# Kernel optimization log

Measured on AMD Instinct MI355X. Metric: run time of the kernel, lower is better.

## Reference

```python
import jax, jax.numpy as jnp
import numpy as np

D = 1024      # neural_dim
M = 8192      # memory_size (assumed fully used)
H = 16        # num_heads
B = 64        # batch
HD = D // H   # head dim


def setup_inputs() -> dict:
    key = jax.random.key(0)
    ks = jax.random.split(key, 24)
    s = 0.02
    inp = {
        "neural_input": jax.random.normal(ks[0], (B, D), jnp.float32),
        "memory_keys": jax.random.normal(ks[1], (M, D), jnp.float32),
        "memory_values": jax.random.normal(ks[2], (M, D), jnp.float32),
        # query/key/value projections (nn.Linear weights are [out, in])
        "Wq": jax.random.normal(ks[3], (D, D), jnp.float32) * s,
        "bq": jnp.zeros((D,), jnp.float32),
        "Wk": jax.random.normal(ks[4], (D, D), jnp.float32) * s,
        "bk": jnp.zeros((D,), jnp.float32),
        "Wv": jax.random.normal(ks[5], (D, D), jnp.float32) * s,
        "bv": jnp.zeros((D,), jnp.float32),
        # MultiheadAttention packed in-projection [3D, D] and out projection
        "in_proj_w": jax.random.normal(ks[6], (3 * D, D), jnp.float32) * s,
        "in_proj_b": jnp.zeros((3 * D,), jnp.float32),
        "out_w": jax.random.normal(ks[7], (D, D), jnp.float32) * s,
        "out_b": jnp.zeros((D,), jnp.float32),
        # memory_gate: Linear(2D->D), ReLU, Linear(D->D), Sigmoid
        "gW1": jax.random.normal(ks[8], (D, 2 * D), jnp.float32) * s,
        "gb1": jnp.zeros((D,), jnp.float32),
        "gW2": jax.random.normal(ks[9], (D, D), jnp.float32) * s,
        "gb2": jnp.zeros((D,), jnp.float32),
        # integration: Linear(2D->2D), ReLU, Linear(2D->D)
        "iW1": jax.random.normal(ks[10], (2 * D, 2 * D), jnp.float32) * s,
        "ib1": jnp.zeros((2 * D,), jnp.float32),
        "iW2": jax.random.normal(ks[11], (D, 2 * D), jnp.float32) * s,
        "ib2": jnp.zeros((D,), jnp.float32),
    }
    return inp


def reference(neural_input, memory_keys, memory_values,
              Wq, bq, Wk, bk, Wv, bv,
              in_proj_w, in_proj_b, out_w, out_b,
              gW1, gb1, gW2, gb2, iW1, ib1, iW2, ib2):
    x = neural_input  # [B, D]
    # pre-projections (memory_used assumed all True -> full tables)
    q = x @ Wq.T + bq                  # [B, D]
    k = memory_keys @ Wk.T + bk        # [M, D]
    v = memory_values @ Wv.T + bv      # [M, D]

    # MultiheadAttention (single query per batch element; K/V shared
    # across batch instead of the redundant expand in the original)
    Wiq, Wik, Wiv = in_proj_w[:D], in_proj_w[D:2 * D], in_proj_w[2 * D:]
    biq, bik, biv = in_proj_b[:D], in_proj_b[D:2 * D], in_proj_b[2 * D:]
    qh = (q @ Wiq.T + biq).reshape(B, H, HD)   # [B, H, hd]
    kh = (k @ Wik.T + bik).reshape(M, H, HD)   # [M, H, hd]
    vh = (v @ Wiv.T + biv).reshape(M, H, HD)   # [M, H, hd]

    scale = 1.0 / np.sqrt(HD).astype(np.float32)
    scores = jnp.einsum('bhd,mhd->bhm', qh, kh) * scale  # [B, H, M]
    attn = jax.nn.softmax(scores, axis=-1)
    ctx = jnp.einsum('bhm,mhd->bhd', attn, vh).reshape(B, D)
    memory_signal = ctx @ out_w.T + out_b      # [B, D]

    # gated fusion
    gate_in = jnp.concatenate([x, memory_signal], axis=-1)          # [B, 2D]
    gate = jax.nn.sigmoid(jax.nn.relu(gate_in @ gW1.T + gb1) @ gW2.T + gb2)
    gated_memory = gate * memory_signal
    combined = jnp.concatenate([x, gated_memory], axis=-1)          # [B, 2D]
    out = jax.nn.relu(combined @ iW1.T + ib1) @ iW2.T + ib2         # [B, D]
    return out
```

## Files before the change

### kernel.cpp

```cpp
#include <hip/hip_runtime.h>
#include <hip/hip_bf16.h>
#include <stdint.h>


typedef __bf16 bf16;
typedef __bf16 bf16x4 __attribute__((ext_vector_type(4)));
typedef __bf16 bf16x8 __attribute__((ext_vector_type(8)));
typedef float f32x4 __attribute__((ext_vector_type(4)));

#define D_ 1024
#define M_ 8192
#define B_ 64
#define H_ 16

static __device__ __forceinline__ void gload16(const void* g, void* l) {
  __builtin_amdgcn_global_load_lds(
      (const __attribute__((address_space(1))) void*)g,
      (__attribute__((address_space(3))) void*)l, 16, 0, 0);
}

struct CvtDesc { const float* src; bf16* dst; int n; int row_len; int row_stride; };
struct CvtArgs { CvtDesc d[10]; };

__global__ __launch_bounds__(256) void cvt_multi(CvtArgs a) {
  CvtDesc dd = a.d[blockIdx.y];
  int i = (blockIdx.x * 256 + threadIdx.x) * 4;
  if (i >= dd.n) return;
  float4 v = *(const float4*)(dd.src + i);
  int r = i / dd.row_len;
  int c = i - r * dd.row_len;
  bf16x4 o = { (bf16)v.x, (bf16)v.y, (bf16)v.z, (bf16)v.w };
  *(bf16x4*)(dd.dst + (int64_t)r * dd.row_stride + c) = o;
}

__global__ __launch_bounds__(256) void transpose_cvt3(
    const float* __restrict__ s0, const float* __restrict__ s1,
    const float* __restrict__ s2, bf16* __restrict__ dst) {
  const float* src = blockIdx.z == 0 ? s0 : blockIdx.z == 1 ? s1 : s2;
  bf16* out = dst + (int64_t)blockIdx.z * D_ * D_;
  __shared__ bf16 tile[32][33];
  int tx = threadIdx.x & 31, ty = threadIdx.x >> 5;
  int r0 = blockIdx.y * 32, c0 = blockIdx.x * 32;
#pragma unroll
  for (int i = 0; i < 32; i += 8)
    tile[ty + i][tx] = (bf16)src[(int64_t)(r0 + ty + i) * D_ + c0 + tx];
  __syncthreads();
#pragma unroll
  for (int i = 0; i < 32; i += 8)
    out[(int64_t)(c0 + ty + i) * D_ + r0 + tx] = tile[tx][ty + i];
}

__global__ __launch_bounds__(256) void transpose_vh(const bf16* __restrict__ in,
                                                    bf16* __restrict__ out) {
  __shared__ bf16 tile[64][66];
  const int t = threadIdx.x;
  const int c0 = blockIdx.x * 64;
  const int r0 = blockIdx.y * 64;
  const int v4 = (t & 15) * 4, rr = t >> 4;
#pragma unroll
  for (int i = 0; i < 64; i += 16) {
    bf16x4 u = *(const bf16x4*)(in + (int64_t)(r0 + rr + i) * D_ + c0 + v4);
    tile[rr + i][v4 + 0] = u.x; tile[rr + i][v4 + 1] = u.y;
    tile[rr + i][v4 + 2] = u.z; tile[rr + i][v4 + 3] = u.w;
  }
  __syncthreads();
#pragma unroll
  for (int i = 0; i < 64; i += 16) {
    int oc = rr + i;
    bf16x4 o = { tile[v4 + 0][oc], tile[v4 + 1][oc],
                 tile[v4 + 2][oc], tile[v4 + 3][oc] };
    *(bf16x4*)(out + (int64_t)(c0 + oc) * M_ + r0 + v4) = o;
  }
}

__global__ __launch_bounds__(256) void bias_combine(
    const float* __restrict__ inw, const float* __restrict__ inb,
    const float* __restrict__ bq, const float* __restrict__ bk,
    const float* __restrict__ bv, float* __restrict__ bc) {
  int z = blockIdx.y, n = blockIdx.x;
  const float* Wi = inw + ((int64_t)z * D_ + n) * D_;
  const float* b = z == 0 ? bq : z == 1 ? bk : bv;
  float acc = 0.f;
  for (int l = threadIdx.x; l < D_; l += 256) acc += Wi[l] * b[l];
#pragma unroll
  for (int m = 32; m; m >>= 1) acc += __shfl_xor(acc, m, 64);
  __shared__ float red[4];
  if ((threadIdx.x & 63) == 0) red[threadIdx.x >> 6] = acc;
  __syncthreads();
  if (threadIdx.x == 0)
    bc[z * D_ + n] = red[0] + red[1] + red[2] + red[3] + inb[z * D_ + n];
}

__global__ __launch_bounds__(256) void gemm_bt_big(
    const bf16* __restrict__ A, int lda, int64_t sA,
    const bf16* __restrict__ Bm, int ldb, int64_t sB,
    bf16* __restrict__ C, int ldc, int64_t sC,
    const float* __restrict__ bias, int64_t sbias, int K) {
  const int z = blockIdx.z;
  A += (int64_t)z * sA; Bm += (int64_t)z * sB; C += (int64_t)z * sC;
  if (bias) bias += (int64_t)z * sbias;
  const int m0 = blockIdx.y * 128, n0 = blockIdx.x * 128;
  __shared__ alignas(16) bf16 As[128 * 32];
  __shared__ alignas(16) bf16 Bs[128 * 32];
  const int tid = threadIdx.x, lane = tid & 63, w = tid >> 6;
  const int wm = (w & 1) * 64, wn = (w >> 1) * 64;
  f32x4 acc[4][4] = {};

  int c0 = w * 64 + lane, c1 = (4 + w) * 64 + lane;
  int ra0 = c0 >> 2, qa0 = (c0 & 3) ^ ((ra0 >> 1) & 3);
  int ra1 = c1 >> 2, qa1 = (c1 & 3) ^ ((ra1 >> 1) & 3);
  const bf16* gA0 = A + (int64_t)(m0 + ra0) * lda + qa0 * 8;
  const bf16* gA1 = A + (int64_t)(m0 + ra1) * lda + qa1 * 8;
  const bf16* gB0 = Bm + (int64_t)(n0 + ra0) * ldb + qa0 * 8;
  const bf16* gB1 = Bm + (int64_t)(n0 + ra1) * ldb + qa1 * 8;
  bf16* lA0 = As + w * 512;
  bf16* lA1 = As + (4 + w) * 512;
  bf16* lB0 = Bs + w * 512;
  bf16* lB1 = Bs + (4 + w) * 512;

  const int rl = lane & 15, qq = lane >> 4;
  for (int k0 = 0; k0 < K; k0 += 32) {
    __syncthreads();
    gload16(gA0 + k0, lA0);
    gload16(gA1 + k0, lA1);
    gload16(gB0 + k0, lB0);
    gload16(gB1 + k0, lB1);
    __syncthreads();
    bf16x8 af[4], bv[4];
#pragma unroll
    for (int i = 0; i < 4; i++) {
      int r = wm + i * 16 + rl;
      af[i] = *(const bf16x8*)(As + r * 32 + (qq ^ ((r >> 1) & 3)) * 8);
    }
#pragma unroll
    for (int j = 0; j < 4; j++) {
      int r = wn + j * 16 + rl;
      bv[j] = *(const bf16x8*)(Bs + r * 32 + (qq ^ ((r >> 1) & 3)) * 8);
    }
#pragma unroll
    for (int i = 0; i < 4; i++)
#pragma unroll
      for (int j = 0; j < 4; j++)
        acc[i][j] = __builtin_amdgcn_mfma_f32_16x16x32_bf16(af[i], bv[j],
                                                            acc[i][j], 0, 0, 0);
  }
#pragma unroll
  for (int j = 0; j < 4; j++) {
    int gn = n0 + wn + j * 16 + rl;
    float bb = bias ? bias[gn] : 0.0f;
#pragma unroll
    for (int i = 0; i < 4; i++) {
      int gm0 = m0 + wm + i * 16 + qq * 4;
#pragma unroll
      for (int r = 0; r < 4; r++)
        C[(int64_t)(gm0 + r) * ldc + gn] = (bf16)(acc[i][j][r] + bb);
    }
  }
}

template <int BK, int EPI, typename OutT>
__global__ __launch_bounds__(256) void gemm_bt_small(
    const bf16* __restrict__ A, int lda, int64_t sA,
    const bf16* __restrict__ Bm, int ldb, int64_t sB,
    OutT* __restrict__ C, int ldc, int64_t sC, int64_t sCk,
    const float* __restrict__ bias, float scale,
    const bf16* __restrict__ aux, int ldaux, int klen) {
  const int z = blockIdx.z, kblk = blockIdx.y;
  A += (int64_t)z * sA + (int64_t)kblk * klen;
  Bm += (int64_t)z * sB + (int64_t)kblk * klen;
  C += (int64_t)z * sC + (int64_t)kblk * sCk;
  const int n0 = blockIdx.x * 64;
  constexpr int CPR = BK / 8;
  constexpr int J = BK / 32;
  __shared__ alignas(16) bf16 As[64 * BK];
  __shared__ alignas(16) bf16 Bs[64 * BK];
  const int tid = threadIdx.x, lane = tid & 63, w = tid >> 6;
  const int rl = lane & 15, qq = lane >> 4;
  f32x4 acc[4] = {};

  const bf16 *gA[J], *gB[J];
  bf16 *lA[J], *lB[J];
#pragma unroll
  for (int j = 0; j < J; j++) {
    int c = (j * 4 + w) * 64 + lane;
    int r = c / CPR, qp = c % CPR;
    int q = qp ^ (r & 7);
    gA[j] = A + (int64_t)r * lda + q * 8;
    gB[j] = Bm + (int64_t)(n0 + r) * ldb + q * 8;
    lA[j] = As + (j * 4 + w) * 512;
    lB[j] = Bs + (j * 4 + w) * 512;
  }
  for (int k0 = 0; k0 < klen; k0 += BK) {
    __syncthreads();
#pragma unroll
    for (int j = 0; j < J; j++) {
      gload16(gA[j] + k0, lA[j]);
      gload16(gB[j] + k0, lB[j]);
    }
    __syncthreads();
#pragma unroll
    for (int kk = 0; kk < BK / 32; kk++) {
      int ar = w * 16 + rl;
      int q = kk * 4 + qq;
      bf16x8 af = *(const bf16x8*)(As + ar * BK + (q ^ (ar & 7)) * 8);
#pragma unroll
      for (int j = 0; j < 4; j++) {
        int br = j * 16 + rl;
        bf16x8 bv = *(const bf16x8*)(Bs + br * BK + (q ^ (br & 7)) * 8);
        acc[j] = __builtin_amdgcn_mfma_f32_16x16x32_bf16(af, bv, acc[j], 0, 0, 0);
      }
    }
  }
#pragma unroll
  for (int j = 0; j < 4; j++) {
    int gn = n0 + j * 16 + rl;
    float bb = bias ? bias[gn] : 0.0f;
#pragma unroll
    for (int r = 0; r < 4; r++) {
      int gm = w * 16 + qq * 4 + r;
      float val = (acc[j][r] + bb) * scale;
      if constexpr (EPI == 1) val = fmaxf(val, 0.0f);
      if constexpr (EPI == 2) {
        float g = 1.0f / (1.0f + __expf(-val));
        val = g * (float)aux[(int64_t)gm * ldaux + gn];
      }
      C[(int64_t)gm * ldc + gn] = (OutT)val;
    }
  }
}

__global__ __launch_bounds__(256) void softmax_kernel(
    const float* __restrict__ scores, bf16* __restrict__ attn) {
  int row = blockIdx.x;
  const float4* s = (const float4*)(scores + (int64_t)row * M_);
  bf16* a = attn + (int64_t)row * M_;
  int t = threadIdx.x;
  float4 v[8];
  float mx = -3.4e38f;
#pragma unroll
  for (int j = 0; j < 8; j++) {
    v[j] = s[j * 256 + t];
    mx = fmaxf(mx, fmaxf(fmaxf(v[j].x, v[j].y), fmaxf(v[j].z, v[j].w)));
  }
#pragma unroll
  for (int m = 32; m; m >>= 1) mx = fmaxf(mx, __shfl_xor(mx, m, 64));
  __shared__ float red[4];
  if ((t & 63) == 0) red[t >> 6] = mx;
  __syncthreads();
  mx = fmaxf(fmaxf(red[0], red[1]), fmaxf(red[2], red[3]));
  float sum = 0.f;
#pragma unroll
  for (int j = 0; j < 8; j++) {
    v[j].x = __expf(v[j].x - mx); v[j].y = __expf(v[j].y - mx);
    v[j].z = __expf(v[j].z - mx); v[j].w = __expf(v[j].w - mx);
    sum += v[j].x + v[j].y + v[j].z + v[j].w;
  }
#pragma unroll
  for (int m = 32; m; m >>= 1) sum += __shfl_xor(sum, m, 64);
  __syncthreads();
  if ((t & 63) == 0) red[t >> 6] = sum;
  __syncthreads();
  sum = red[0] + red[1] + red[2] + red[3];
  float rinv = 1.0f / sum;
#pragma unroll
  for (int j = 0; j < 8; j++) {
    bf16x4 o = { (bf16)(v[j].x * rinv), (bf16)(v[j].y * rinv),
                 (bf16)(v[j].z * rinv), (bf16)(v[j].w * rinv) };
    *(bf16x4*)(a + (int64_t)(j * 256 + t) * 4) = o;
  }
}

__global__ __launch_bounds__(256) void ctx_reduce(const float* __restrict__ part,
                                                  bf16* __restrict__ ctx) {
  int t = blockIdx.x * 256 + threadIdx.x;
  int h = t >> 12, b = (t >> 6) & 63, d = t & 63;
  float s = 0.f;
#pragma unroll
  for (int ks = 0; ks < 8; ks++)
    s += part[((int64_t)(h * 8 + ks) * 64 + b) * 64 + d];
  ctx[(int64_t)b * D_ + h * 64 + d] = (bf16)s;
}

extern "C" void kernel_launch(void* const* d_in, const int* in_sizes, int n_in,
                              void* d_out, int out_size, void* d_ws,
                              size_t ws_size, hipStream_t stream) {
  (void)in_sizes; (void)n_in; (void)out_size;
  const float* x    = (const float*)d_in[0];
  const float* mk   = (const float*)d_in[1];
  const float* mv   = (const float*)d_in[2];
  const float* Wq   = (const float*)d_in[3];
  const float* bq   = (const float*)d_in[4];
  const float* Wk   = (const float*)d_in[5];
  const float* bk   = (const float*)d_in[6];
  const float* Wv   = (const float*)d_in[7];
  const float* bv   = (const float*)d_in[8];
  const float* inw  = (const float*)d_in[9];
  const float* inb  = (const float*)d_in[10];
  const float* outw = (const float*)d_in[11];
  const float* outb = (const float*)d_in[12];
  const float* gW1  = (const float*)d_in[13];
  const float* gb1  = (const float*)d_in[14];
  const float* gW2  = (const float*)d_in[15];
  const float* gb2  = (const float*)d_in[16];
  const float* iW1  = (const float*)d_in[17];
  const float* ib1  = (const float*)d_in[18];
  const float* iW2  = (const float*)d_in[19];
  const float* ib2  = (const float*)d_in[20];

  char* ws = (char*)d_ws;
  size_t off = 0;
  auto alloc = [&](size_t bytes) {
    char* p = ws + off;
    off += (bytes + 255) & ~(size_t)255;
    return p;
  };
  bf16* mkmv  = (bf16*)alloc((size_t)2 * M_ * D_ * 2);
  bf16* inpj  = (bf16*)alloc((size_t)3 * D_ * D_ * 2);
  bf16* WT    = (bf16*)alloc((size_t)3 * D_ * D_ * 2);
  bf16* Wc    = (bf16*)alloc((size_t)3 * D_ * D_ * 2);
  float* bc   = (float*)alloc(3 * D_ * 4);
  bf16* xms   = (bf16*)alloc((size_t)B_ * 2 * D_ * 2);
  bf16* xgm   = (bf16*)alloc((size_t)B_ * 2 * D_ * 2);
  bf16* qh    = (bf16*)alloc((size_t)B_ * D_ * 2);
  bf16* khvh  = (bf16*)alloc((size_t)2 * M_ * D_ * 2);
  bf16* vhT   = (bf16*)alloc((size_t)M_ * D_ * 2);
  bf16* attn  = (bf16*)alloc((size_t)H_ * B_ * M_ * 2);
  float* part = (float*)alloc((size_t)16 * 8 * 64 * 64 * 4);
  bf16* ctx   = (bf16*)alloc((size_t)B_ * D_ * 2);
  bf16* g1    = (bf16*)alloc((size_t)B_ * D_ * 2);
  bf16* h1    = (bf16*)alloc((size_t)B_ * 2 * D_ * 2);
  bf16* gW1b  = (bf16*)alloc((size_t)D_ * 2 * D_ * 2);
  bf16* gW2b  = (bf16*)alloc((size_t)D_ * D_ * 2);
  bf16* iW1b  = (bf16*)alloc((size_t)2 * D_ * 2 * D_ * 2);
  bf16* iW2b  = (bf16*)alloc((size_t)D_ * 2 * D_ * 2);
  bf16* outwb = (bf16*)alloc((size_t)D_ * D_ * 2);
  float* scores = (float*)mkmv;
  if (ws_size < off) return;

  CvtArgs ca;
  ca.d[0] = { mk,  mkmv,            M_ * D_,     M_ * D_,     M_ * D_ };
  ca.d[1] = { mv,  mkmv + M_ * D_,  M_ * D_,     M_ * D_,     M_ * D_ };
  ca.d[2] = { inw, inpj,            3 * D_ * D_, 3 * D_ * D_, 3 * D_ * D_ };
  ca.d[3] = { gW1, gW1b,            D_ * 2 * D_, D_ * 2 * D_, D_ * 2 * D_ };
  ca.d[4] = { gW2, gW2b,            D_ * D_,     D_ * D_,     D_ * D_ };
  ca.d[5] = { iW1, iW1b,        2 * D_ * 2 * D_, 2 * D_ * 2 * D_, 2 * D_ * 2 * D_ };
  ca.d[6] = { iW2, iW2b,            D_ * 2 * D_, D_ * 2 * D_, D_ * 2 * D_ };
  ca.d[7] = { outw, outwb,          D_ * D_,     D_ * D_,     D_ * D_ };
  ca.d[8] = { x,   xms,             B_ * D_,     D_,          2 * D_ };
  ca.d[9] = { x,   xgm,             B_ * D_,     D_,          2 * D_ };
  cvt_multi<<<dim3(8192, 10), 256, 0, stream>>>(ca);

  transpose_cvt3<<<dim3(32, 32, 3), 256, 0, stream>>>(Wq, Wk, Wv, WT);

  bias_combine<<<dim3(D_, 3), 256, 0, stream>>>(inw, inb, bq, bk, bv, bc);

  gemm_bt_big<<<dim3(8, 8, 3), 256, 0, stream>>>(
      inpj, D_, (int64_t)D_ * D_, WT, D_, (int64_t)D_ * D_,
      Wc, D_, (int64_t)D_ * D_, nullptr, 0, D_);

  gemm_bt_big<<<dim3(8, 64, 2), 256, 0, stream>>>(
      mkmv, D_, (int64_t)M_ * D_, Wc + (int64_t)D_ * D_, D_, (int64_t)D_ * D_,
      khvh, D_, (int64_t)M_ * D_, bc + D_, D_, D_);

  gemm_bt_small<128, 0, bf16><<<dim3(16, 1, 1), 256, 0, stream>>>(
      xms, 2 * D_, 0, Wc, D_, 0, qh, D_, 0, 0, bc, 0.125f, nullptr, 0, D_);

  gemm_bt_small<64, 0, float><<<dim3(128, 1, 16), 256, 0, stream>>>(
      qh, D_, 64, khvh, D_, 64, scores, M_, (int64_t)B_ * M_, 0,
      nullptr, 1.0f, nullptr, 0, 64);

  softmax_kernel<<<dim3(H_ * B_), 256, 0, stream>>>(scores, attn);

  transpose_vh<<<dim3(16, 128), 256, 0, stream>>>(khvh + (int64_t)M_ * D_, vhT);

  gemm_bt_small<128, 0, float><<<dim3(1, 8, 16), 256, 0, stream>>>(
      attn, M_, (int64_t)B_ * M_, vhT, M_, (int64_t)64 * M_,
      part, 64, (int64_t)8 * 4096, 4096, nullptr, 1.0f, nullptr, 0, 1024);
  ctx_reduce<<<dim3(256), 256, 0, stream>>>(part, ctx);

  gemm_bt_small<128, 0, bf16><<<dim3(16, 1, 1), 256, 0, stream>>>(
      ctx, D_, 0, outwb, D_, 0, xms + D_, 2 * D_, 0, 0, outb, 1.0f,
      nullptr, 0, D_);

  gemm_bt_small<128, 1, bf16><<<dim3(16, 1, 1), 256, 0, stream>>>(
      xms, 2 * D_, 0, gW1b, 2 * D_, 0, g1, D_, 0, 0, gb1, 1.0f,
      nullptr, 0, 2 * D_);

  gemm_bt_small<128, 2, bf16><<<dim3(16, 1, 1), 256, 0, stream>>>(
      g1, D_, 0, gW2b, D_, 0, xgm + D_, 2 * D_, 0, 0, gb2, 1.0f,
      xms + D_, 2 * D_, D_);

  gemm_bt_small<128, 1, bf16><<<dim3(32, 1, 1), 256, 0, stream>>>(
      xgm, 2 * D_, 0, iW1b, 2 * D_, 0, h1, 2 * D_, 0, 0, ib1, 1.0f,
      nullptr, 0, 2 * D_);

  gemm_bt_small<128, 0, float><<<dim3(16, 1, 1), 256, 0, stream>>>(
      h1, 2 * D_, 0, iW2b, 2 * D_, 0, (float*)d_out, D_, 0, 0, ib2, 1.0f,
      nullptr, 0, 2 * D_);
}
```

Baseline: 412.6 us.

## Fuse V transpose into projection GEMM, flatten conversion, drop LDS in thin GEMMs

```diff
diff --git a/kernel.cpp b/kernel.cpp
--- a/kernel.cpp
+++ b/kernel.cpp
@@ -19,18 +19,22 @@
       (__attribute__((address_space(3))) void*)l, 16, 0, 0);
 }
 
-struct CvtDesc { const float* src; bf16* dst; int n; int row_len; int row_stride; };
-struct CvtArgs { CvtDesc d[10]; };
-
-__global__ __launch_bounds__(256) void cvt_multi(CvtArgs a) {
-  CvtDesc dd = a.d[blockIdx.y];
-  int i = (blockIdx.x * 256 + threadIdx.x) * 4;
-  if (i >= dd.n) return;
+struct CvtD { const float* src; bf16* dst; int end; int shift; int stride; };
+struct CvtA { CvtD d[10]; };
+
+__global__ __launch_bounds__(256) void cvt_flat(CvtA a) {
+  int g = blockIdx.x * 256 + threadIdx.x;
+  CvtD dd = a.d[9];
+  int begin = a.d[8].end;
+#pragma unroll
+  for (int t = 8; t >= 0; t--)
+    if (g < a.d[t].end) { dd = a.d[t]; begin = t ? a.d[t - 1].end : 0; }
+  int i = (g - begin) * 4;
   float4 v = *(const float4*)(dd.src + i);
-  int r = i / dd.row_len;
-  int c = i - r * dd.row_len;
+  int r = i >> dd.shift;
+  int c = i - (r << dd.shift);
   bf16x4 o = { (bf16)v.x, (bf16)v.y, (bf16)v.z, (bf16)v.w };
-  *(bf16x4*)(dd.dst + (int64_t)r * dd.row_stride + c) = o;
+  *(bf16x4*)(dd.dst + (int64_t)r * dd.stride + c) = o;
 }
 
 __global__ __launch_bounds__(256) void transpose_cvt3(
@@ -48,29 +52,6 @@
 #pragma unroll
   for (int i = 0; i < 32; i += 8)
     out[(int64_t)(c0 + ty + i) * D_ + r0 + tx] = tile[tx][ty + i];
-}
-
-__global__ __launch_bounds__(256) void transpose_vh(const bf16* __restrict__ in,
-                                                    bf16* __restrict__ out) {
-  __shared__ bf16 tile[64][66];
-  const int t = threadIdx.x;
-  const int c0 = blockIdx.x * 64;
-  const int r0 = blockIdx.y * 64;
-  const int v4 = (t & 15) * 4, rr = t >> 4;
-#pragma unroll
-  for (int i = 0; i < 64; i += 16) {
-    bf16x4 u = *(const bf16x4*)(in + (int64_t)(r0 + rr + i) * D_ + c0 + v4);
-    tile[rr + i][v4 + 0] = u.x; tile[rr + i][v4 + 1] = u.y;
-    tile[rr + i][v4 + 2] = u.z; tile[rr + i][v4 + 3] = u.w;
-  }
-  __syncthreads();
-#pragma unroll
-  for (int i = 0; i < 64; i += 16) {
-    int oc = rr + i;
-    bf16x4 o = { tile[v4 + 0][oc], tile[v4 + 1][oc],
-                 tile[v4 + 2][oc], tile[v4 + 3][oc] };
-    *(bf16x4*)(out + (int64_t)(c0 + oc) * M_ + r0 + v4) = o;
-  }
 }
 
 __global__ __launch_bounds__(256) void bias_combine(
@@ -91,15 +72,24 @@
     bc[z * D_ + n] = red[0] + red[1] + red[2] + red[3] + inb[z * D_ + n];
 }
 
-__global__ __launch_bounds__(256) void gemm_bt_big(
+template <int MODE>
+__global__ __launch_bounds__(256) void gemm_big(
     const bf16* __restrict__ A, int lda, int64_t sA,
     const bf16* __restrict__ Bm, int ldb, int64_t sB,
-    bf16* __restrict__ C, int ldc, int64_t sC,
+    bf16* __restrict__ C, int ldc, int64_t sC, bf16* __restrict__ Ct,
     const float* __restrict__ bias, int64_t sbias, int K) {
-  const int z = blockIdx.z;
-  A += (int64_t)z * sA; Bm += (int64_t)z * sB; C += (int64_t)z * sC;
+  int m0, n0, z;
+  if (MODE == 0) {
+    z = blockIdx.z; m0 = blockIdx.y * 128; n0 = blockIdx.x * 128;
+  } else {
+    int lin = blockIdx.x, xcd = lin & 7, slot = lin >> 3;
+    z = slot >> 6;
+    int r = slot & 63;
+    m0 = (xcd * 8 + (r >> 3)) * 128;
+    n0 = (r & 7) * 128;
+  }
+  A += (int64_t)z * sA; Bm += (int64_t)z * sB;
   if (bias) bias += (int64_t)z * sbias;
-  const int m0 = blockIdx.y * 128, n0 = blockIdx.x * 128;
   __shared__ alignas(16) bf16 As[128 * 32];
   __shared__ alignas(16) bf16 Bs[128 * 32];
   const int tid = threadIdx.x, lane = tid & 63, w = tid >> 6;
@@ -144,22 +134,39 @@
         acc[i][j] = __builtin_amdgcn_mfma_f32_16x16x32_bf16(af[i], bv[j],
                                                             acc[i][j], 0, 0, 0);
   }
-#pragma unroll
-  for (int j = 0; j < 4; j++) {
-    int gn = n0 + wn + j * 16 + rl;
-    float bb = bias ? bias[gn] : 0.0f;
-#pragma unroll
-    for (int i = 0; i < 4; i++) {
-      int gm0 = m0 + wm + i * 16 + qq * 4;
-#pragma unroll
-      for (int r = 0; r < 4; r++)
-        C[(int64_t)(gm0 + r) * ldc + gn] = (bf16)(acc[i][j][r] + bb);
-    }
-  }
-}
-
-template <int BK, int EPI, typename OutT>
-__global__ __launch_bounds__(256) void gemm_bt_small(
+  if (MODE == 1 && z == 1) {
+#pragma unroll
+    for (int j = 0; j < 4; j++) {
+      int gn = n0 + wn + j * 16 + rl;
+      float bb = bias ? bias[gn] : 0.0f;
+#pragma unroll
+      for (int i = 0; i < 4; i++) {
+        int gm0 = m0 + wm + i * 16 + qq * 4;
+        f32x4 a = acc[i][j];
+        bf16x4 o = { (bf16)(a[0] + bb), (bf16)(a[1] + bb),
+                     (bf16)(a[2] + bb), (bf16)(a[3] + bb) };
+        *(bf16x4*)(Ct + (int64_t)gn * M_ + gm0) = o;
+      }
+    }
+  } else {
+    C += (int64_t)z * sC;
+#pragma unroll
+    for (int j = 0; j < 4; j++) {
+      int gn = n0 + wn + j * 16 + rl;
+      float bb = bias ? bias[gn] : 0.0f;
+#pragma unroll
+      for (int i = 0; i < 4; i++) {
+        int gm0 = m0 + wm + i * 16 + qq * 4;
+#pragma unroll
+        for (int r = 0; r < 4; r++)
+          C[(int64_t)(gm0 + r) * ldc + gn] = (bf16)(acc[i][j][r] + bb);
+      }
+    }
+  }
+}
+
+template <int UNROLL, int EPI, typename OutT>
+__global__ __launch_bounds__(256) void gemm_thin(
     const bf16* __restrict__ A, int lda, int64_t sA,
     const bf16* __restrict__ Bm, int ldb, int64_t sB,
     OutT* __restrict__ C, int ldc, int64_t sC, int64_t sCk,
@@ -170,46 +177,31 @@
   Bm += (int64_t)z * sB + (int64_t)kblk * klen;
   C += (int64_t)z * sC + (int64_t)kblk * sCk;
   const int n0 = blockIdx.x * 64;
-  constexpr int CPR = BK / 8;
-  constexpr int J = BK / 32;
-  __shared__ alignas(16) bf16 As[64 * BK];
-  __shared__ alignas(16) bf16 Bs[64 * BK];
   const int tid = threadIdx.x, lane = tid & 63, w = tid >> 6;
   const int rl = lane & 15, qq = lane >> 4;
+  const bf16* pa = A + (int64_t)(w * 16 + rl) * lda + qq * 8;
+  const bf16* pb0 = Bm + (int64_t)(n0 + rl) * ldb + qq * 8;
+  const bf16* pb1 = pb0 + (int64_t)16 * ldb;
+  const bf16* pb2 = pb0 + (int64_t)32 * ldb;
+  const bf16* pb3 = pb0 + (int64_t)48 * ldb;
   f32x4 acc[4] = {};
-
-  const bf16 *gA[J], *gB[J];
-  bf16 *lA[J], *lB[J];
-#pragma unroll
-  for (int j = 0; j < J; j++) {
-    int c = (j * 4 + w) * 64 + lane;
-    int r = c / CPR, qp = c % CPR;
-    int q = qp ^ (r & 7);
-    gA[j] = A + (int64_t)r * lda + q * 8;
-    gB[j] = Bm + (int64_t)(n0 + r) * ldb + q * 8;
-    lA[j] = As + (j * 4 + w) * 512;
-    lB[j] = Bs + (j * 4 + w) * 512;
-  }
-  for (int k0 = 0; k0 < klen; k0 += BK) {
-    __syncthreads();
-#pragma unroll
-    for (int j = 0; j < J; j++) {
-      gload16(gA[j] + k0, lA[j]);
-      gload16(gB[j] + k0, lB[j]);
-    }
-    __syncthreads();
-#pragma unroll
-    for (int kk = 0; kk < BK / 32; kk++) {
-      int ar = w * 16 + rl;
-      int q = kk * 4 + qq;
-      bf16x8 af = *(const bf16x8*)(As + ar * BK + (q ^ (ar & 7)) * 8);
-#pragma unroll
-      for (int j = 0; j < 4; j++) {
-        int br = j * 16 + rl;
-        bf16x8 bv = *(const bf16x8*)(Bs + br * BK + (q ^ (br & 7)) * 8);
-        acc[j] = __builtin_amdgcn_mfma_f32_16x16x32_bf16(af, bv, acc[j], 0, 0, 0);
-      }
-    }
+  for (int k0 = 0; k0 < klen; k0 += 32 * UNROLL) {
+    bf16x8 av[UNROLL], bv[UNROLL][4];
+#pragma unroll
+    for (int u = 0; u < UNROLL; u++) {
+      int k = k0 + u * 32;
+      av[u] = *(const bf16x8*)(pa + k);
+      bv[u][0] = *(const bf16x8*)(pb0 + k);
+      bv[u][1] = *(const bf16x8*)(pb1 + k);
+      bv[u][2] = *(const bf16x8*)(pb2 + k);
+      bv[u][3] = *(const bf16x8*)(pb3 + k);
+    }
+#pragma unroll
+    for (int u = 0; u < UNROLL; u++)
+#pragma unroll
+      for (int j = 0; j < 4; j++)
+        acc[j] = __builtin_amdgcn_mfma_f32_16x16x32_bf16(av[u], bv[u][j],
+                                                         acc[j], 0, 0, 0);
   }
 #pragma unroll
   for (int j = 0; j < 4; j++) {
@@ -337,64 +329,62 @@
   float* scores = (float*)mkmv;
   if (ws_size < off) return;
 
-  CvtArgs ca;
-  ca.d[0] = { mk,  mkmv,            M_ * D_,     M_ * D_,     M_ * D_ };
-  ca.d[1] = { mv,  mkmv + M_ * D_,  M_ * D_,     M_ * D_,     M_ * D_ };
-  ca.d[2] = { inw, inpj,            3 * D_ * D_, 3 * D_ * D_, 3 * D_ * D_ };
-  ca.d[3] = { gW1, gW1b,            D_ * 2 * D_, D_ * 2 * D_, D_ * 2 * D_ };
-  ca.d[4] = { gW2, gW2b,            D_ * D_,     D_ * D_,     D_ * D_ };
-  ca.d[5] = { iW1, iW1b,        2 * D_ * 2 * D_, 2 * D_ * 2 * D_, 2 * D_ * 2 * D_ };
-  ca.d[6] = { iW2, iW2b,            D_ * 2 * D_, D_ * 2 * D_, D_ * 2 * D_ };
-  ca.d[7] = { outw, outwb,          D_ * D_,     D_ * D_,     D_ * D_ };
-  ca.d[8] = { x,   xms,             B_ * D_,     D_,          2 * D_ };
-  ca.d[9] = { x,   xgm,             B_ * D_,     D_,          2 * D_ };
-  cvt_multi<<<dim3(8192, 10), 256, 0, stream>>>(ca);
+  CvtA ca;
+  ca.d[0] = { mk,   mkmv,           2097152, 30, 0 };
+  ca.d[1] = { mv,   mkmv + M_ * D_, 4194304, 30, 0 };
+  ca.d[2] = { inw,  inpj,           4980736, 30, 0 };
+  ca.d[3] = { gW1,  gW1b,           5505024, 30, 0 };
+  ca.d[4] = { gW2,  gW2b,           5767168, 30, 0 };
+  ca.d[5] = { iW1,  iW1b,           6815744, 30, 0 };
+  ca.d[6] = { iW2,  iW2b,           7340032, 30, 0 };
+  ca.d[7] = { outw, outwb,          7602176, 30, 0 };
+  ca.d[8] = { x,    xms,            7618560, 10, 2 * D_ };
+  ca.d[9] = { x,    xgm,            7634944, 10, 2 * D_ };
+  cvt_flat<<<dim3(29824), 256, 0, stream>>>(ca);
 
   transpose_cvt3<<<dim3(32, 32, 3), 256, 0, stream>>>(Wq, Wk, Wv, WT);
 
   bias_combine<<<dim3(D_, 3), 256, 0, stream>>>(inw, inb, bq, bk, bv, bc);
 
-  gemm_bt_big<<<dim3(8, 8, 3), 256, 0, stream>>>(
+  gemm_big<0><<<dim3(8, 8, 3), 256, 0, stream>>>(
       inpj, D_, (int64_t)D_ * D_, WT, D_, (int64_t)D_ * D_,
-      Wc, D_, (int64_t)D_ * D_, nullptr, 0, D_);
-
-  gemm_bt_big<<<dim3(8, 64, 2), 256, 0, stream>>>(
+      Wc, D_, (int64_t)D_ * D_, nullptr, nullptr, 0, D_);
+
+  gemm_big<1><<<dim3(1024), 256, 0, stream>>>(
       mkmv, D_, (int64_t)M_ * D_, Wc + (int64_t)D_ * D_, D_, (int64_t)D_ * D_,
-      khvh, D_, (int64_t)M_ * D_, bc + D_, D_, D_);
-
-  gemm_bt_small<128, 0, bf16><<<dim3(16, 1, 1), 256, 0, stream>>>(
+      khvh, D_, (int64_t)M_ * D_, vhT, bc + D_, D_, D_);
+
+  gemm_thin<4, 0, bf16><<<dim3(16, 1, 1), 256, 0, stream>>>(
       xms, 2 * D_, 0, Wc, D_, 0, qh, D_, 0, 0, bc, 0.125f, nullptr, 0, D_);
 
-  gemm_bt_small<64, 0, float><<<dim3(128, 1, 16), 256, 0, stream>>>(
+  gemm_thin<2, 0, float><<<dim3(128, 1, 16), 256, 0, stream>>>(
       qh, D_, 64, khvh, D_, 64, scores, M_, (int64_t)B_ * M_, 0,
       nullptr, 1.0f, nullptr, 0, 64);
 
   softmax_kernel<<<dim3(H_ * B_), 256, 0, stream>>>(scores, attn);
 
-  transpose_vh<<<dim3(16, 128), 256, 0, stream>>>(khvh + (int64_t)M_ * D_, vhT);
-
-  gemm_bt_small<128, 0, float><<<dim3(1, 8, 16), 256, 0, stream>>>(
+  gemm_thin<4, 0, float><<<dim3(1, 8, 16), 256, 0, stream>>>(
       attn, M_, (int64_t)B_ * M_, vhT, M_, (int64_t)64 * M_,
       part, 64, (int64_t)8 * 4096, 4096, nullptr, 1.0f, nullptr, 0, 1024);
   ctx_reduce<<<dim3(256), 256, 0, stream>>>(part, ctx);
 
-  gemm_bt_small<128, 0, bf16><<<dim3(16, 1, 1), 256, 0, stream>>>(
+  gemm_thin<4, 0, bf16><<<dim3(16, 1, 1), 256, 0, stream>>>(
       ctx, D_, 0, outwb, D_, 0, xms + D_, 2 * D_, 0, 0, outb, 1.0f,
       nullptr, 0, D_);
 
-  gemm_bt_small<128, 1, bf16><<<dim3(16, 1, 1), 256, 0, stream>>>(
+  gemm_thin<4, 1, bf16><<<dim3(16, 1, 1), 256, 0, stream>>>(
       xms, 2 * D_, 0, gW1b, 2 * D_, 0, g1, D_, 0, 0, gb1, 1.0f,
       nullptr, 0, 2 * D_);
 
-  gemm_bt_small<128, 2, bf16><<<dim3(16, 1, 1), 256, 0, stream>>>(
+  gemm_thin<4, 2, bf16><<<dim3(16, 1, 1), 256, 0, stream>>>(
       g1, D_, 0, gW2b, D_, 0, xgm + D_, 2 * D_, 0, 0, gb2, 1.0f,
       xms + D_, 2 * D_, D_);
 
-  gemm_bt_small<128, 1, bf16><<<dim3(32, 1, 1), 256, 0, stream>>>(
+  gemm_thin<4, 1, bf16><<<dim3(32, 1, 1), 256, 0, stream>>>(
       xgm, 2 * D_, 0, iW1b, 2 * D_, 0, h1, 2 * D_, 0, 0, ib1, 1.0f,
       nullptr, 0, 2 * D_);
 
-  gemm_bt_small<128, 0, float><<<dim3(16, 1, 1), 256, 0, stream>>>(
+  gemm_thin<4, 0, float><<<dim3(16, 1, 1), 256, 0, stream>>>(
       h1, 2 * D_, 0, iW2b, 2 * D_, 0, (float*)d_out, D_, 0, 0, ib2, 1.0f,
       nullptr, 0, 2 * D_);
 }
```

New measurement: 519.5 us. 1.26x slower.
